# Optimization experiments

Measured on AMD Instinct MI355X. Metric: run time of the kernel, lower is better.

## Reference

```python
import jax, jax.numpy as jnp
import numpy as np

T, B, D, H = 1024, 256, 128, 256

def setup_inputs() -> dict:
    key = jax.random.key(0)
    ks = jax.random.split(key, 6)
    s = 1.0 / np.sqrt(H)
    return {
        "x": jax.random.normal(ks[0], (T, B, D), dtype=jnp.float32),
        "delta_ts": jax.random.uniform(ks[1], (B, T), dtype=jnp.float32) * 10.0,  # elapsed times > 0
        "h0": jnp.zeros((B, H), dtype=jnp.float32),
        "c0": jnp.zeros((B, H), dtype=jnp.float32),
        "W": jax.random.normal(ks[2], (4 * H, D), dtype=jnp.float32) * s,
        "U": jax.random.normal(ks[3], (4 * H, H), dtype=jnp.float32) * s,
        "b": jnp.zeros((4 * H,), dtype=jnp.float32),
        "Wd": jax.random.normal(ks[4], (H, H), dtype=jnp.float32) * s,
        "bd": jnp.zeros((H,), dtype=jnp.float32),
    }

def reference(x, delta_ts, h0, c0, W, U, b, Wd, bd):
    """Time-aware LSTM (T-LSTM, Baytas et al. 2017) layer over time-major input.
    x: [T,B,D], delta_ts: [B,T]. Returns (outputs [T,B,H], (h,c))."""
    e = jnp.float32(np.e)

    def step(carry, inp):
        h, c = carry                 # [B,H] each
        xt, dt = inp                 # [B,D], [B]
        # memory decomposition with elapsed-time discount g(dt)=1/log(e+dt)
        Cs = jnp.tanh(c @ Wd.T + bd)                     # short-term memory [B,H]
        Cs_hat = Cs * (1.0 / jnp.log(e + dt))[:, None]   # discounted short-term
        c_star = c - Cs + Cs_hat                          # adjusted previous cell
        gates = xt @ W.T + h @ U.T + b                    # [B,4H]
        i, f, g, o = jnp.split(gates, 4, axis=-1)
        c_new = jax.nn.sigmoid(f) * c_star + jax.nn.sigmoid(i) * jnp.tanh(g)
        h_new = jax.nn.sigmoid(o) * jnp.tanh(c_new)
        return (h_new, c_new), h_new

    (h, c), outs = jax.lax.scan(step, (h0, c0), (x, delta_ts.T))
    return outs, h, c
```

## Files before the change

### kernel.cpp

```cpp
#include <hip/hip_runtime.h>

#define T_STEPS 1024
#define BATCH   256
#define DIM     128
#define HID     256
#define NSLICE  8
#define BT      16
#define NGROUP  (BATCH / BT)
#define NBLOCK  (NGROUP * NSLICE)
#define JW      (HID / NSLICE)

#define U_OFF    0
#define W_OFF    65536
#define WD_OFF   98304
#define H_OFF    114688
#define C_OFF    122880
#define GST_OFF  131072
#define CS0_OFF  139520
#define CS1_OFF  141632
#define SMEM_TOTAL 143744

typedef float f32x4 __attribute__((ext_vector_type(4)));
typedef short bf16x8 __attribute__((ext_vector_type(8)));

__device__ __forceinline__ unsigned short f2bf(float f) {
    union { float f; unsigned u; } v; v.f = f;
    unsigned r = (v.u + 0x7fffu + ((v.u >> 16) & 1u)) >> 16;
    return (unsigned short)r;
}
__device__ __forceinline__ float sigm(float v) { return 1.0f / (1.0f + __expf(-v)); }
__device__ __forceinline__ float tanh_fast(float v) {
    const float e = __expf(2.0f * v);
    return 1.0f - 2.0f / (e + 1.0f);
}

#define FLAG_IDX(g, s, w) (((g) * 8 + (s)) * 32 + (w))

__global__ __launch_bounds__(512)
void tlstm_kernel(const float* __restrict__ x,
                  const float* __restrict__ dts,
                  const float* __restrict__ h0,
                  const float* __restrict__ c0,
                  const float* __restrict__ W,
                  const float* __restrict__ U,
                  const float* __restrict__ bvec,
                  const float* __restrict__ Wd,
                  const float* __restrict__ bd,
                  float* __restrict__ out,
                  unsigned int* flags,
                  unsigned int* hb32,
                  unsigned int* cb32)
{
    extern __shared__ char smem[];
    float* gates_st = (float*)(smem + GST_OFF);
    float* cs0      = (float*)(smem + CS0_OFF);
    float* cs1      = (float*)(smem + CS1_OFF);

    const int tid = threadIdx.x;
    const int g  = blockIdx.x / NSLICE;
    const int s  = blockIdx.x % NSLICE;
    const int bb = g * BT;
    const int jb = s * JW;

    const int lane = tid & 63;
    const int wid  = tid >> 6;
    const int lrow = lane & 15;
    const int lkg  = lane >> 4;
    const int n0   = wid << 4;

    const int b_ = tid >> 5;
    const int jj = tid & 31;

    for (int idx = tid; idx < 128 * 256; idx += 512) {
        const int r = idx >> 8, k = idx & 255;
        const int urow = ((r >> 5) * HID) + jb + (r & 31);
        int bo = (r << 9) + (k << 1); bo ^= (r & 7) << 4;
        *(unsigned short*)(smem + U_OFF + bo) = f2bf(U[(size_t)urow * HID + k]);
    }
    for (int idx = tid; idx < 128 * 128; idx += 512) {
        const int r = idx >> 7, k = idx & 127;
        const int wrow = ((r >> 5) * HID) + jb + (r & 31);
        int bo = (r << 8) + (k << 1); bo ^= (r & 7) << 4;
        *(unsigned short*)(smem + W_OFF + bo) = f2bf(W[(size_t)wrow * DIM + k]);
    }
    for (int idx = tid; idx < 32 * 256; idx += 512) {
        const int r = idx >> 8, k = idx & 255;
        int bo = (r << 9) + (k << 1); bo ^= (r & 7) << 4;
        *(unsigned short*)(smem + WD_OFF + bo) = f2bf(Wd[(size_t)(jb + r) * HID + k]);
    }

    const float bI = bvec[jb + jj];
    const float bF = bvec[HID + jb + jj];
    const float bG = bvec[2 * HID + jb + jj];
    const float bO = bvec[3 * HID + jb + jj];
    const float bD = bd[jb + jj];

    float4 xr[8];
    float dt_cur;
    {
        const float* xp = x + ((size_t)0 * BATCH + bb + lrow) * DIM + (lkg << 3);
        #pragma unroll
        for (int kc = 0; kc < 4; ++kc) {
            xr[2 * kc]     = *(const float4*)(xp + kc * 32);
            xr[2 * kc + 1] = *(const float4*)(xp + kc * 32 + 4);
        }
        dt_cur = dts[(size_t)(bb + b_) * T_STEPS + 0];
    }

    float c_reg;
    {
        const float h0v = h0[(size_t)(bb + b_) * HID + jb + jj];
        const float c0v = c0[(size_t)(bb + b_) * HID + jb + jj];
        c_reg = c0v;
        const unsigned short hb16 = f2bf(h0v), cb16 = f2bf(c0v);
        const int oh = __shfl_xor((int)hb16, 1);
        const int oc = __shfl_xor((int)cb16, 1);
        if ((jj & 1) == 0) {
            const unsigned int hw = (unsigned)hb16 | ((unsigned)oh << 16);
            const unsigned int cw = (unsigned)cb16 | ((unsigned)oc << 16);
            const int ei = (((0 * NGROUP + g) * 8 + s) * 16 + b_) * 16 + (jj >> 1);
            __hip_atomic_store(hb32 + ei, hw, __ATOMIC_RELAXED, __HIP_MEMORY_SCOPE_AGENT);
            __hip_atomic_store(cb32 + ei, cw, __ATOMIC_RELAXED, __HIP_MEMORY_SCOPE_AGENT);
        }
    }
    asm volatile("s_waitcnt vmcnt(0)" ::: "memory");
    if (lane == 0)
        __hip_atomic_store(flags + FLAG_IDX(g, s, wid), 1u,
                           __ATOMIC_RELAXED, __HIP_MEMORY_SCOPE_AGENT);

    for (int t = 0; t < T_STEPS; ++t) {
        const int cur = t & 1;

        bf16x8 xa[4];
        #pragma unroll
        for (int kc = 0; kc < 4; ++kc) {
            const float4 f0 = xr[2 * kc];
            const float4 f1 = xr[2 * kc + 1];
            bf16x8 a;
            a[0] = (short)f2bf(f0.x); a[1] = (short)f2bf(f0.y);
            a[2] = (short)f2bf(f0.z); a[3] = (short)f2bf(f0.w);
            a[4] = (short)f2bf(f1.x); a[5] = (short)f2bf(f1.y);
            a[6] = (short)f2bf(f1.z); a[7] = (short)f2bf(f1.w);
            xa[kc] = a;
        }
        f32x4 accX = {0.f, 0.f, 0.f, 0.f};
        {
            const int wr = n0 + lrow;
            #pragma unroll
            for (int kc = 0; kc < 4; ++kc) {
                int wo = (wr << 8) + ((kc * 32 + (lkg << 3)) << 1); wo ^= (wr & 7) << 4;
                const bf16x8 wv = *(const bf16x8*)(smem + W_OFF + wo);
                accX = __builtin_amdgcn_mfma_f32_16x16x32_bf16(xa[kc], wv, accX, 0, 0, 0);
            }
        }

        {
            const unsigned target = (unsigned)(t + 1);
            const unsigned* fb = flags + FLAG_IDX(g, wid, 0);
            unsigned fl = target;
            do {
                if (lane < 8)
                    fl = __hip_atomic_load(fb + lane, __ATOMIC_RELAXED, __HIP_MEMORY_SCOPE_AGENT);
            } while (__any((int)(fl < target)));
        }
        asm volatile("" ::: "memory");
        __builtin_amdgcn_sched_barrier(0);

        {
            const int boff = ((cur * NGROUP + g) * 8 + wid) * 256;
            const unsigned long long* hq = (const unsigned long long*)(hb32 + boff);
            const unsigned long long* cq = (const unsigned long long*)(cb32 + boff);
            const unsigned long long h1 = __hip_atomic_load(hq + lane,      __ATOMIC_RELAXED, __HIP_MEMORY_SCOPE_AGENT);
            const unsigned long long h2 = __hip_atomic_load(hq + lane + 64, __ATOMIC_RELAXED, __HIP_MEMORY_SCOPE_AGENT);
            const unsigned long long c1 = __hip_atomic_load(cq + lane,      __ATOMIC_RELAXED, __HIP_MEMORY_SCOPE_AGENT);
            const unsigned long long c2 = __hip_atomic_load(cq + lane + 64, __ATOMIC_RELAXED, __HIP_MEMORY_SCOPE_AGENT);
            const int r1 = lane >> 3, r2 = 8 + (lane >> 3);
            const int cb = (wid << 6) + ((lane & 7) << 3);
            int bo1 = (r1 << 9) + cb; bo1 ^= (r1 & 7) << 4;
            int bo2 = (r2 << 9) + cb; bo2 ^= (r2 & 7) << 4;
            *(unsigned long long*)(smem + H_OFF + bo1) = h1;
            *(unsigned long long*)(smem + H_OFF + bo2) = h2;
            *(unsigned long long*)(smem + C_OFF + bo1) = c1;
            *(unsigned long long*)(smem + C_OFF + bo2) = c2;
        }
        __syncthreads();

        f32x4 accH = {0.f, 0.f, 0.f, 0.f};
        {
            const int wr = n0 + lrow;
            #pragma unroll
            for (int kc = 0; kc < 8; ++kc) {
                int ao = (lrow << 9) + ((kc * 32 + (lkg << 3)) << 1); ao ^= (lrow & 7) << 4;
                const bf16x8 av = *(const bf16x8*)(smem + H_OFF + ao);
                int uo = (wr << 9) + ((kc * 32 + (lkg << 3)) << 1); uo ^= (wr & 7) << 4;
                const bf16x8 uv = *(const bf16x8*)(smem + U_OFF + uo);
                accH = __builtin_amdgcn_mfma_f32_16x16x32_bf16(av, uv, accH, 0, 0, 0);
            }
        }
        if (wid < 4) {
            f32x4 accC = {0.f, 0.f, 0.f, 0.f};
            const int nt = wid >> 1;
            const int kh = wid & 1;
            const int wr = (nt << 4) + lrow;
            #pragma unroll
            for (int kc = 0; kc < 4; ++kc) {
                const int kk = kh * 4 + kc;
                int ao = (lrow << 9) + ((kk * 32 + (lkg << 3)) << 1); ao ^= (lrow & 7) << 4;
                const bf16x8 av = *(const bf16x8*)(smem + C_OFF + ao);
                int wo = (wr << 9) + ((kk * 32 + (lkg << 3)) << 1); wo ^= (wr & 7) << 4;
                const bf16x8 wv = *(const bf16x8*)(smem + WD_OFF + wo);
                accC = __builtin_amdgcn_mfma_f32_16x16x32_bf16(av, wv, accC, 0, 0, 0);
            }
            float* dst = kh ? cs1 : cs0;
            #pragma unroll
            for (int i = 0; i < 4; ++i)
                dst[((lkg << 2) + i) * 33 + (nt << 4) + lrow] = accC[i];
        }
        #pragma unroll
        for (int i = 0; i < 4; ++i)
            gates_st[((lkg << 2) + i) * 132 + n0 + lrow] = accX[i] + accH[i];

        __syncthreads();

        float cn, hn;
        {
            const float ipre = gates_st[b_ * 132 + jj]      + bI;
            const float fpre = gates_st[b_ * 132 + 32 + jj] + bF;
            const float gpre = gates_st[b_ * 132 + 64 + jj] + bG;
            const float opre = gates_st[b_ * 132 + 96 + jj] + bO;
            const float cspre = cs0[b_ * 33 + jj] + cs1[b_ * 33 + jj] + bD;
            const float gdt  = 1.0f / __logf(2.718281828459045f + dt_cur);
            const float Cs    = tanh_fast(cspre);
            const float cstar = c_reg - Cs + Cs * gdt;
            cn = sigm(fpre) * cstar + sigm(ipre) * tanh_fast(gpre);
            hn = sigm(opre) * tanh_fast(cn);
            c_reg = cn;
        }

        if (t == T_STEPS - 1) {
            out[((size_t)t * BATCH + bb + b_) * HID + jb + jj] = hn;
            const size_t base = (size_t)T_STEPS * BATCH * HID;
            out[base + (size_t)(bb + b_) * HID + jb + jj] = hn;
            out[base + (size_t)BATCH * HID + (size_t)(bb + b_) * HID + jb + jj] = cn;
            break;
        }

        {
            const unsigned short hb16 = f2bf(hn), cb16 = f2bf(cn);
            const int oh = __shfl_xor((int)hb16, 1);
            const int oc = __shfl_xor((int)cb16, 1);
            if ((jj & 1) == 0) {
                const unsigned int hw = (unsigned)hb16 | ((unsigned)oh << 16);
                const unsigned int cw = (unsigned)cb16 | ((unsigned)oc << 16);
                const int ei = ((((cur ^ 1) * NGROUP + g) * 8 + s) * 16 + b_) * 16 + (jj >> 1);
                __hip_atomic_store(hb32 + ei, hw, __ATOMIC_RELAXED, __HIP_MEMORY_SCOPE_AGENT);
                __hip_atomic_store(cb32 + ei, cw, __ATOMIC_RELAXED, __HIP_MEMORY_SCOPE_AGENT);
            }
        }
        asm volatile("s_waitcnt vmcnt(0)" ::: "memory");
        if (lane == 0)
            __hip_atomic_store(flags + FLAG_IDX(g, s, wid), (unsigned)(t + 2),
                               __ATOMIC_RELAXED, __HIP_MEMORY_SCOPE_AGENT);

        out[((size_t)t * BATCH + bb + b_) * HID + jb + jj] = hn;
        {
            const float* xp = x + ((size_t)(t + 1) * BATCH + bb + lrow) * DIM + (lkg << 3);
            #pragma unroll
            for (int kc = 0; kc < 4; ++kc) {
                xr[2 * kc]     = *(const float4*)(xp + kc * 32);
                xr[2 * kc + 1] = *(const float4*)(xp + kc * 32 + 4);
            }
            dt_cur = dts[(size_t)(bb + b_) * T_STEPS + (t + 1)];
        }
    }
}

extern "C" void kernel_launch(void* const* d_in, const int* in_sizes, int n_in,
                              void* d_out, int out_size, void* d_ws, size_t ws_size,
                              hipStream_t stream) {
    (void)in_sizes; (void)n_in; (void)out_size; (void)ws_size;
    const float* x   = (const float*)d_in[0];
    const float* dts = (const float*)d_in[1];
    const float* h0  = (const float*)d_in[2];
    const float* c0  = (const float*)d_in[3];
    const float* W   = (const float*)d_in[4];
    const float* U   = (const float*)d_in[5];
    const float* bv  = (const float*)d_in[6];
    const float* Wd  = (const float*)d_in[7];
    const float* bd  = (const float*)d_in[8];
    float* out = (float*)d_out;

    char* ws = (char*)d_ws;
    unsigned int* flags = (unsigned int*)ws;
    unsigned int* hb32  = (unsigned int*)(ws + 16384);
    unsigned int* cb32  = (unsigned int*)(ws + 16384 + 262144);

    hipMemsetAsync(flags, 0, 16384, stream);
    hipFuncSetAttribute((const void*)tlstm_kernel,
                        hipFuncAttributeMaxDynamicSharedMemorySize, SMEM_TOTAL);
    tlstm_kernel<<<dim3(NBLOCK), dim3(512), SMEM_TOTAL, stream>>>(
        x, dts, h0, c0, W, U, bv, Wd, bd, out, flags, hb32, cb32);
}
```

Measured before the change: 4.821 ms.

## Replace flag-based handoff with step-tagged 64-bit h/c exchange words

```diff
diff --git a/kernel.cpp b/kernel.cpp
--- a/kernel.cpp
+++ b/kernel.cpp
@@ -33,8 +33,6 @@
     const float e = __expf(2.0f * v);
     return 1.0f - 2.0f / (e + 1.0f);
 }
-
-#define FLAG_IDX(g, s, w) (((g) * 8 + (s)) * 32 + (w))
 
 __global__ __launch_bounds__(512)
 void tlstm_kernel(const float* __restrict__ x,
@@ -47,9 +45,7 @@
                   const float* __restrict__ Wd,
                   const float* __restrict__ bd,
                   float* __restrict__ out,
-                  unsigned int* flags,
-                  unsigned int* hb32,
-                  unsigned int* cb32)
+                  unsigned long long* pbuf)
 {
     extern __shared__ char smem[];
     float* gates_st = (float*)(smem + GST_OFF);
@@ -112,21 +108,11 @@
         const float h0v = h0[(size_t)(bb + b_) * HID + jb + jj];
         const float c0v = c0[(size_t)(bb + b_) * HID + jb + jj];
         c_reg = c0v;
-        const unsigned short hb16 = f2bf(h0v), cb16 = f2bf(c0v);
-        const int oh = __shfl_xor((int)hb16, 1);
-        const int oc = __shfl_xor((int)cb16, 1);
-        if ((jj & 1) == 0) {
-            const unsigned int hw = (unsigned)hb16 | ((unsigned)oh << 16);
-            const unsigned int cw = (unsigned)cb16 | ((unsigned)oc << 16);
-            const int ei = (((0 * NGROUP + g) * 8 + s) * 16 + b_) * 16 + (jj >> 1);
-            __hip_atomic_store(hb32 + ei, hw, __ATOMIC_RELAXED, __HIP_MEMORY_SCOPE_AGENT);
-            __hip_atomic_store(cb32 + ei, cw, __ATOMIC_RELAXED, __HIP_MEMORY_SCOPE_AGENT);
-        }
-    }
-    asm volatile("s_waitcnt vmcnt(0)" ::: "memory");
-    if (lane == 0)
-        __hip_atomic_store(flags + FLAG_IDX(g, s, wid), 1u,
-                           __ATOMIC_RELAXED, __HIP_MEMORY_SCOPE_AGENT);
+        const unsigned long long pv = (1ull << 32)
+            | ((unsigned)f2bf(h0v) << 16) | (unsigned)f2bf(c0v);
+        const size_t ei = (((size_t)0 * NGROUP + g) * NSLICE + s) * 512 + b_ * 32 + jj;
+        __hip_atomic_store(pbuf + ei, pv, __ATOMIC_RELAXED, __HIP_MEMORY_SCOPE_AGENT);
+    }
 
     for (int t = 0; t < T_STEPS; ++t) {
         const int cur = t & 1;
@@ -154,34 +140,36 @@
             }
         }
 
+        unsigned long long v[8];
         {
             const unsigned target = (unsigned)(t + 1);
-            const unsigned* fb = flags + FLAG_IDX(g, wid, 0);
-            unsigned fl = target;
+            const unsigned long long* sp = pbuf
+                + (((size_t)cur * NGROUP + g) * NSLICE + wid) * 512
+                + ((lane >> 2) * 32 + ((lane & 3) << 3));
+            bool ok;
             do {
-                if (lane < 8)
-                    fl = __hip_atomic_load(fb + lane, __ATOMIC_RELAXED, __HIP_MEMORY_SCOPE_AGENT);
-            } while (__any((int)(fl < target)));
-        }
-        asm volatile("" ::: "memory");
-        __builtin_amdgcn_sched_barrier(0);
-
-        {
-            const int boff = ((cur * NGROUP + g) * 8 + wid) * 256;
-            const unsigned long long* hq = (const unsigned long long*)(hb32 + boff);
-            const unsigned long long* cq = (const unsigned long long*)(cb32 + boff);
-            const unsigned long long h1 = __hip_atomic_load(hq + lane,      __ATOMIC_RELAXED, __HIP_MEMORY_SCOPE_AGENT);
-            const unsigned long long h2 = __hip_atomic_load(hq + lane + 64, __ATOMIC_RELAXED, __HIP_MEMORY_SCOPE_AGENT);
-            const unsigned long long c1 = __hip_atomic_load(cq + lane,      __ATOMIC_RELAXED, __HIP_MEMORY_SCOPE_AGENT);
-            const unsigned long long c2 = __hip_atomic_load(cq + lane + 64, __ATOMIC_RELAXED, __HIP_MEMORY_SCOPE_AGENT);
-            const int r1 = lane >> 3, r2 = 8 + (lane >> 3);
-            const int cb = (wid << 6) + ((lane & 7) << 3);
-            int bo1 = (r1 << 9) + cb; bo1 ^= (r1 & 7) << 4;
-            int bo2 = (r2 << 9) + cb; bo2 ^= (r2 & 7) << 4;
-            *(unsigned long long*)(smem + H_OFF + bo1) = h1;
-            *(unsigned long long*)(smem + H_OFF + bo2) = h2;
-            *(unsigned long long*)(smem + C_OFF + bo1) = c1;
-            *(unsigned long long*)(smem + C_OFF + bo2) = c2;
+                #pragma unroll
+                for (int i = 0; i < 8; ++i)
+                    v[i] = __hip_atomic_load(sp + i, __ATOMIC_RELAXED, __HIP_MEMORY_SCOPE_AGENT);
+                ok = true;
+                #pragma unroll
+                for (int i = 0; i < 8; ++i)
+                    ok = ok && ((unsigned)(v[i] >> 32) == target);
+            } while (!__all((int)ok));
+        }
+
+        {
+            bf16x8 hv, cv;
+            #pragma unroll
+            for (int i = 0; i < 8; ++i) {
+                hv[i] = (short)((unsigned short)(v[i] >> 16));
+                cv[i] = (short)((unsigned short)(v[i] & 0xffffu));
+            }
+            const int r  = lane >> 2;
+            const int cb = (wid << 6) + ((lane & 3) << 4);
+            int bo = (r << 9) + cb; bo ^= (r & 7) << 4;
+            *(bf16x8*)(smem + H_OFF + bo) = hv;
+            *(bf16x8*)(smem + C_OFF + bo) = cv;
         }
         __syncthreads();
 
@@ -246,21 +234,12 @@
         }
 
         {
-            const unsigned short hb16 = f2bf(hn), cb16 = f2bf(cn);
-            const int oh = __shfl_xor((int)hb16, 1);
-            const int oc = __shfl_xor((int)cb16, 1);
-            if ((jj & 1) == 0) {
-                const unsigned int hw = (unsigned)hb16 | ((unsigned)oh << 16);
-                const unsigned int cw = (unsigned)cb16 | ((unsigned)oc << 16);
-                const int ei = ((((cur ^ 1) * NGROUP + g) * 8 + s) * 16 + b_) * 16 + (jj >> 1);
-                __hip_atomic_store(hb32 + ei, hw, __ATOMIC_RELAXED, __HIP_MEMORY_SCOPE_AGENT);
-                __hip_atomic_store(cb32 + ei, cw, __ATOMIC_RELAXED, __HIP_MEMORY_SCOPE_AGENT);
-            }
-        }
-        asm volatile("s_waitcnt vmcnt(0)" ::: "memory");
-        if (lane == 0)
-            __hip_atomic_store(flags + FLAG_IDX(g, s, wid), (unsigned)(t + 2),
-                               __ATOMIC_RELAXED, __HIP_MEMORY_SCOPE_AGENT);
+            const unsigned long long pv = ((unsigned long long)(unsigned)(t + 2) << 32)
+                | ((unsigned)f2bf(hn) << 16) | (unsigned)f2bf(cn);
+            const size_t ei = (((size_t)(cur ^ 1) * NGROUP + g) * NSLICE + s) * 512
+                            + b_ * 32 + jj;
+            __hip_atomic_store(pbuf + ei, pv, __ATOMIC_RELAXED, __HIP_MEMORY_SCOPE_AGENT);
+        }
 
         out[((size_t)t * BATCH + bb + b_) * HID + jb + jj] = hn;
         {
@@ -290,14 +269,12 @@
     const float* bd  = (const float*)d_in[8];
     float* out = (float*)d_out;
 
-    char* ws = (char*)d_ws;
-    unsigned int* flags = (unsigned int*)ws;
-    unsigned int* hb32  = (unsigned int*)(ws + 16384);
-    unsigned int* cb32  = (unsigned int*)(ws + 16384 + 262144);
-
-    hipMemsetAsync(flags, 0, 16384, stream);
+    unsigned long long* pbuf = (unsigned long long*)d_ws;
+    const size_t pbuf_bytes = 2ull * NGROUP * NSLICE * 512 * 8;
+
+    hipMemsetAsync(pbuf, 0, pbuf_bytes, stream);
     hipFuncSetAttribute((const void*)tlstm_kernel,
                         hipFuncAttributeMaxDynamicSharedMemorySize, SMEM_TOTAL);
     tlstm_kernel<<<dim3(NBLOCK), dim3(512), SMEM_TOTAL, stream>>>(
-        x, dts, h0, c0, W, U, bv, Wd, bd, out, flags, hb32, cb32);
-}
+        x, dts, h0, c0, W, U, bv, Wd, bd, out, pbuf);
+}
```

After: 5.439 ms. 1.13x slower.
